# Optimization experiments

Hardware: AMD Instinct MI355X
Metric: run time of the kernel (lower is better)

The kernel has to match this reference:

```python
import jax, jax.numpy as jnp
import numpy as np

FP8_MAX = 448.0  # finfo(float8_e4m3fn).max
BLK = 128        # block_size = [128, 128]


def _quant_dequant_act(x):
    """Dynamic per-token, per-128-block fp8 quantization followed by dequant.
    Matches fp8_act_quant: scale = amax(block)/448, q = fp8(x/scale), deq = q*scale."""
    T, K = x.shape
    xb = x.reshape(T, K // BLK, BLK)
    amax = jnp.max(jnp.abs(xb), axis=-1, keepdims=True)
    scale = jnp.maximum(amax, 1e-12) / FP8_MAX  # [T, K//BLK, 1]
    q = (xb / scale).astype(jnp.float8_e4m3fn).astype(jnp.float32)
    return (q * scale).reshape(T, K)


def _dequant_weight(w, s):
    """Block-wise dequant of an fp8-valued [N, K] weight with [N//BLK, K//BLK] scales."""
    N, K = w.shape
    wb = w.reshape(N // BLK, BLK, K // BLK, BLK)
    return (wb * s[:, None, :, None]).reshape(N, K)


def setup_inputs() -> dict:
    key = jax.random.key(0)
    ks = jax.random.split(key, 7)
    T, H, I, E, TOPK = 8192, 2048, 1024, 32, 8
    f8 = lambda x: x.astype(jnp.float8_e4m3fn).astype(jnp.float32)  # store fp8-valued weights as f32
    hidden_states = jax.random.normal(ks[0], (T, H), jnp.float32)
    gate_up_proj = f8(jax.random.normal(ks[1], (E, 2 * I, H), jnp.float32))
    gate_up_proj_scale_inv = jax.random.uniform(ks[2], (E, (2 * I) // BLK, H // BLK), jnp.float32, 0.005, 0.02)
    down_proj = f8(jax.random.normal(ks[3], (E, H, I), jnp.float32))
    down_proj_scale_inv = jax.random.uniform(ks[4], (E, H // BLK, I // BLK), jnp.float32, 0.005, 0.02)
    top_k_index = jax.random.randint(ks[5], (T, TOPK), 0, E, jnp.int32)
    tw = jax.random.uniform(ks[6], (T, TOPK), jnp.float32)
    top_k_weights = tw / jnp.sum(tw, axis=-1, keepdims=True)
    return {
        'hidden_states': hidden_states,
        'gate_up_proj': gate_up_proj,
        'gate_up_proj_scale_inv': gate_up_proj_scale_inv,
        'down_proj': down_proj,
        'down_proj_scale_inv': down_proj_scale_inv,
        'top_k_weights': top_k_weights,
        'top_k_index': top_k_index,
    }


def reference(hidden_states, gate_up_proj, gate_up_proj_scale_inv, down_proj,
              down_proj_scale_inv, top_k_weights, top_k_index):
    E = gate_up_proj.shape[0]
    # Dynamic activation quantization is per-token (expert-independent): do it once.
    x_deq = _quant_dequant_act(hidden_states)  # [T, H]
    # Per-expert combine weight: cw[e, t] = sum_k top_k_weights[t,k] * (top_k_index[t,k]==e)
    hit = top_k_index[None, :, :] == jnp.arange(E, dtype=top_k_index.dtype)[:, None, None]
    cw = jnp.sum(jnp.where(hit, top_k_weights[None, :, :], 0.0), axis=-1)  # [E, T]

    def body(acc, xs):
        wgu, sgu, wd, sd, w_tok = xs
        h = x_deq @ _dequant_weight(wgu, sgu).T          # [T, 2I] fp8 grouped GEMM
        gate, up = jnp.split(h, 2, axis=-1)
        h = jax.nn.silu(gate) * up                        # _apply_gate
        h = _quant_dequant_act(h)                         # re-quantize before down_proj
        y = h @ _dequant_weight(wd, sd).T                 # [T, H]
        return acc + w_tok[:, None] * y, None

    acc0 = jnp.zeros_like(hidden_states, dtype=jnp.float32)
    out, _ = jax.lax.scan(
        body, acc0,
        (gate_up_proj, gate_up_proj_scale_inv, down_proj, down_proj_scale_inv, cw))
    return out
```

## Files before the change

### kernel.cpp

```cpp
#include <hip/hip_runtime.h>

typedef float f32x4 __attribute__((ext_vector_type(4)));
typedef float f32x16 __attribute__((ext_vector_type(16)));
typedef long long i64t;

constexpr int T = 8192, H = 2048, II = 1024, E = 32, TOPK = 8;
constexpr int NSLOT = T * TOPK;
constexpr int MT_MAX = 32;
constexpr int MT1 = 64;

__device__ __forceinline__ i64t frag8(const unsigned char* lds, int row, int kbyte) {
  int c8 = (kbyte >> 3) ^ ((row & 7) << 1) ^ ((row >> 3) & 1);
  return *(const i64t*)(lds + row * 128 + c8 * 8);
}
__device__ __forceinline__ void wr16c(unsigned char* lds, int r, int c, uint4 v) {
  if ((r >> 3) & 1) v = make_uint4(v.z, v.w, v.x, v.y);
  *(uint4*)(lds + r * 128 + ((c ^ (r & 7)) << 4)) = v;
}

__global__ void k_quant_x(const float* __restrict__ x, unsigned char* __restrict__ x8,
                          float* __restrict__ xs) {
  int gw = blockIdx.x * 4 + (threadIdx.x >> 6);
  int lane = threadIdx.x & 63;
  int token = gw >> 4, kb = gw & 15;
  float2 v = *(const float2*)(x + (size_t)token * H + kb * 128 + lane * 2);
  float am = fmaxf(fabsf(v.x), fabsf(v.y));
#pragma unroll
  for (int m = 1; m <= 32; m <<= 1) am = fmaxf(am, __shfl_xor(am, m, 64));
  float scale = fmaxf(am, 1e-12f) / 448.0f;
  int pk = __builtin_amdgcn_cvt_pk_fp8_f32(v.x / scale, v.y / scale, 0, false);
  *(unsigned short*)(x8 + (size_t)token * H + kb * 128 + lane * 2) = (unsigned short)(pk & 0xffff);
  if (lane == 0) xs[token * 16 + kb] = scale;
}

__global__ void k_cvt_w(const float* __restrict__ w, unsigned char* __restrict__ w8, int n4) {
  int i = blockIdx.x * 256 + threadIdx.x;
  if (i >= n4) return;
  f32x4 v = *(const f32x4*)(w + (size_t)i * 4);
  int p = __builtin_amdgcn_cvt_pk_fp8_f32(v[0], v[1], 0, false);
  p = __builtin_amdgcn_cvt_pk_fp8_f32(v[2], v[3], p, true);
  *(unsigned int*)(w8 + (size_t)i * 4) = (unsigned int)p;
}

__global__ void k_count(const int* __restrict__ tki, int* __restrict__ counts) {
  int i = blockIdx.x * 256 + threadIdx.x;
  if (i < NSLOT) atomicAdd(&counts[tki[i]], 1);
}
__global__ void k_scan(const int* __restrict__ counts, int* __restrict__ offsets) {
  if (threadIdx.x == 0) {
    int s = 0;
    for (int e = 0; e < E; ++e) { offsets[e] = s; s += counts[e]; }
    offsets[E] = s;
  }
}
__global__ void k_fill(const int* __restrict__ tki, const float* __restrict__ tkw,
                       const int* __restrict__ offsets, int* __restrict__ cursor,
                       int* __restrict__ tok_list, float* __restrict__ cw_list) {
  int i = blockIdx.x * 256 + threadIdx.x;
  if (i < NSLOT) {
    int e = tki[i];
    int pos = atomicAdd(&cursor[e], 1);
    int slot = offsets[e] + pos;
    tok_list[slot] = i >> 3;
    cw_list[slot] = tkw[i];
  }
}

__launch_bounds__(256, 2)
__global__ void k_gemm1(const unsigned char* __restrict__ x8, const float* __restrict__ xs,
                        const unsigned char* __restrict__ wgu8, const float* __restrict__ sgu,
                        const int* __restrict__ offsets, const int* __restrict__ tok_list,
                        unsigned char* __restrict__ a8, float* __restrict__ ascale) {
  __shared__ __align__(16) unsigned char lA[64 * 128];
  __shared__ __align__(16) unsigned char lBg[128 * 128];
  __shared__ __align__(16) unsigned char lBu[128 * 128];
  __shared__ float lsx[16 * 64];
  __shared__ int ltok[64];
  __shared__ float lamax[64 * 2];
  __shared__ float lscale[64];

  int bx = blockIdx.x;
  int e = bx >> 9, mt = (bx >> 3) & 63, nt = bx & 7;
  int off0 = offsets[e];
  int Me = offsets[e + 1] - off0;
  if (mt * 64 >= Me) return;
  int vrows = Me - mt * 64; if (vrows > 64) vrows = 64;
  int tid = threadIdx.x;

  if (tid < 64) ltok[tid] = (tid < vrows) ? tok_list[off0 + mt * 64 + tid] : -1;
  __syncthreads();

  if (tid < 128) {
    int r = tid >> 1, h = tid & 1;
    int tokr = ltok[r]; int tk = tokr < 0 ? 0 : tokr;
#pragma unroll
    for (int i = 0; i < 2; ++i) {
      f32x4 v = *(const f32x4*)(xs + (size_t)tk * 16 + h * 8 + i * 4);
#pragma unroll
      for (int j = 0; j < 4; ++j) lsx[(h * 8 + i * 4 + j) * 64 + r] = (tokr < 0) ? 0.0f : v[j];
    }
  }

  const int lane = tid & 63, wid = tid >> 6;
  const int wm = wid >> 1, wn = wid & 1;
  const int l31 = lane & 31, lg = lane >> 5;

  const int ra = tid >> 2, qa = tid & 3;
  const int rb = tid >> 1, hb = tid & 1;
  int tokA = ltok[ra] < 0 ? 0 : ltok[ra];
  const unsigned char* gA = x8 + (size_t)tokA * H + qa * 32;
  const unsigned char* gG = wgu8 + ((size_t)e * 2048 + nt * 128 + rb) * H + hb * 64;
  const unsigned char* gU = gG + (size_t)1024 * H;

  {
    uint4 a0 = *(const uint4*)gA, a1 = *(const uint4*)(gA + 16);
    uint4 g0 = *(const uint4*)gG, g1 = *(const uint4*)(gG + 16);
    uint4 g2 = *(const uint4*)(gG + 32), g3 = *(const uint4*)(gG + 48);
    uint4 u0 = *(const uint4*)gU, u1 = *(const uint4*)(gU + 16);
    uint4 u2 = *(const uint4*)(gU + 32), u3 = *(const uint4*)(gU + 48);
    wr16c(lA, ra, qa * 2 + 0, a0); wr16c(lA, ra, qa * 2 + 1, a1);
    wr16c(lBg, rb, hb * 4 + 0, g0); wr16c(lBg, rb, hb * 4 + 1, g1);
    wr16c(lBg, rb, hb * 4 + 2, g2); wr16c(lBg, rb, hb * 4 + 3, g3);
    wr16c(lBu, rb, hb * 4 + 0, u0); wr16c(lBu, rb, hb * 4 + 1, u1);
    wr16c(lBu, rb, hb * 4 + 2, u2); wr16c(lBu, rb, hb * 4 + 3, u3);
  }
  __syncthreads();

  f32x16 aG[2] = {};
  f32x16 aU[2] = {};

  for (int kb = 0; kb < 16; ++kb) {
    uint4 pA0, pA1, pG0, pG1, pG2, pG3, pU0, pU1, pU2, pU3;
    if (kb < 15) {
      pA0 = *(const uint4*)(gA + (kb + 1) * 128);
      pA1 = *(const uint4*)(gA + (kb + 1) * 128 + 16);
      pG0 = *(const uint4*)(gG + (kb + 1) * 128);
      pG1 = *(const uint4*)(gG + (kb + 1) * 128 + 16);
      pG2 = *(const uint4*)(gG + (kb + 1) * 128 + 32);
      pG3 = *(const uint4*)(gG + (kb + 1) * 128 + 48);
      pU0 = *(const uint4*)(gU + (kb + 1) * 128);
      pU1 = *(const uint4*)(gU + (kb + 1) * 128 + 16);
      pU2 = *(const uint4*)(gU + (kb + 1) * 128 + 32);
      pU3 = *(const uint4*)(gU + (kb + 1) * 128 + 48);
    }

    float swg = sgu[(e * 16 + nt) * 16 + kb];
    float swu = sgu[(e * 16 + 8 + nt) * 16 + kb];

    i64t af[8];
#pragma unroll
    for (int ks = 0; ks < 8; ++ks)
      af[ks] = frag8(lA, wm * 32 + l31, ks * 16 + lg * 8);
    f32x4 sxv[4];
#pragma unroll
    for (int jj = 0; jj < 4; ++jj)
      sxv[jj] = *(const f32x4*)(&lsx[kb * 64 + wm * 32 + jj * 8 + lg * 4]);

#pragma unroll
    for (int gu = 0; gu < 2; ++gu) {
      const unsigned char* lB = gu ? lBu : lBg;
      float sw = gu ? swu : swg;
#pragma unroll
      for (int nf = 0; nf < 2; ++nf) {
        i64t bf[8];
#pragma unroll
        for (int ks = 0; ks < 8; ++ks)
          bf[ks] = frag8(lB, wn * 64 + nf * 32 + l31, ks * 16 + lg * 8);
        f32x16 t = {};
#pragma unroll
        for (int ks = 0; ks < 8; ++ks)
          t = __builtin_amdgcn_mfma_f32_32x32x16_fp8_fp8(af[ks], bf[ks], t, 0, 0, 0);
#pragma unroll
        for (int j = 0; j < 16; ++j) {
          float f = sxv[j >> 2][j & 3] * sw;
          if (gu) aU[nf][j] += t[j] * f; else aG[nf][j] += t[j] * f;
        }
      }
    }

    if (kb < 15) {
      __syncthreads();
      wr16c(lA, ra, qa * 2 + 0, pA0); wr16c(lA, ra, qa * 2 + 1, pA1);
      wr16c(lBg, rb, hb * 4 + 0, pG0); wr16c(lBg, rb, hb * 4 + 1, pG1);
      wr16c(lBg, rb, hb * 4 + 2, pG2); wr16c(lBg, rb, hb * 4 + 3, pG3);
      wr16c(lBu, rb, hb * 4 + 0, pU0); wr16c(lBu, rb, hb * 4 + 1, pU1);
      wr16c(lBu, rb, hb * 4 + 2, pU2); wr16c(lBu, rb, hb * 4 + 3, pU3);
      __syncthreads();
    }
  }

#pragma unroll
  for (int nf = 0; nf < 2; ++nf)
#pragma unroll
    for (int j = 0; j < 16; ++j) {
      float g = aG[nf][j], u = aU[nf][j];
      aG[nf][j] = g * (1.0f / (1.0f + expf(-g))) * u;
    }

#pragma unroll
  for (int j = 0; j < 16; ++j) {
    float m = fmaxf(fabsf(aG[0][j]), fabsf(aG[1][j]));
#pragma unroll
    for (int msk = 1; msk <= 16; msk <<= 1) m = fmaxf(m, __shfl_xor(m, msk, 64));
    if (l31 == 0)
      lamax[(wm * 32 + (j & 3) + ((j >> 2) * 8) + lg * 4) * 2 + wn] = m;
  }
  __syncthreads();
  if (tid < 64) {
    float mm = fmaxf(lamax[tid * 2], lamax[tid * 2 + 1]);
    lscale[tid] = fmaxf(mm, 1e-12f) / 448.0f;
  }
  __syncthreads();

#pragma unroll
  for (int j = 0; j < 16; ++j) {
    int row = wm * 32 + (j & 3) + ((j >> 2) * 8) + lg * 4;
    float sc = lscale[row];
#pragma unroll
    for (int nf = 0; nf < 2; ++nf) {
      int pk = __builtin_amdgcn_cvt_pk_fp8_f32(aG[nf][j] / sc, 0.0f, 0, false);
      lA[row * 128 + wn * 64 + nf * 32 + l31] = (unsigned char)(pk & 0xff);
    }
    if (row < vrows && l31 == 0 && wn == 0)
      ascale[(off0 + mt * 64 + row) * 8 + nt] = sc;
  }
  __syncthreads();
#pragma unroll
  for (int it = 0; it < 2; ++it) {
    int idx = it * 256 + tid;
    int row = idx >> 3, c = idx & 7;
    if (row < vrows)
      *(uint4*)(a8 + (size_t)(off0 + mt * 64 + row) * 1024 + nt * 128 + c * 16) =
          *(const uint4*)(lA + row * 128 + c * 16);
  }
}

__launch_bounds__(256, 2)
__global__ void k_gemm2(const unsigned char* __restrict__ a8, const float* __restrict__ ascale,
                        const unsigned char* __restrict__ wd8, const float* __restrict__ sd,
                        const int* __restrict__ offsets, const int* __restrict__ tok_list,
                        const float* __restrict__ cw_list, float* __restrict__ out) {
  __shared__ __align__(16) unsigned char lA[128 * 128];
  __shared__ __align__(16) unsigned char lB[128 * 128];
  __shared__ float las[8 * 128];
  __shared__ int ltok[128];
  __shared__ float lcw[128];

  int bx = blockIdx.x;
  int e = bx >> 9, mt = (bx >> 4) & 31, nt = bx & 15;
  int off0 = offsets[e];
  int Me = offsets[e + 1] - off0;
  if (mt * 128 >= Me) return;
  int vrows = Me - mt * 128; if (vrows > 128) vrows = 128;
  int tid = threadIdx.x;

  if (tid < 128) {
    bool v = tid < vrows;
    ltok[tid] = v ? tok_list[off0 + mt * 128 + tid] : 0;
    lcw[tid] = v ? cw_list[off0 + mt * 128 + tid] : 0.0f;
  }
  int r = tid >> 1, h = tid & 1;
  int srow = off0 + mt * 128 + r; if (srow > NSLOT - 1) srow = NSLOT - 1;
  {
    f32x4 v = *(const f32x4*)(ascale + (size_t)srow * 8 + h * 4);
#pragma unroll
    for (int j = 0; j < 4; ++j) las[(h * 4 + j) * 128 + r] = v[j];
  }

  const int lane = tid & 63, wid = tid >> 6;
  const int wm = wid >> 1, wn = wid & 1;
  const int l31 = lane & 31, lg = lane >> 5;

  const unsigned char* gA = a8 + (size_t)srow * 1024 + h * 64;
  const unsigned char* gB = wd8 + ((size_t)e * 2048 + nt * 128 + r) * 1024 + h * 64;

  uint4 rA[4], rB[4];
#pragma unroll
  for (int i = 0; i < 4; ++i) { rA[i] = ((const uint4*)gA)[i]; rB[i] = ((const uint4*)gB)[i]; }
#pragma unroll
  for (int i = 0; i < 4; ++i) { wr16c(lA, r, h * 4 + i, rA[i]); wr16c(lB, r, h * 4 + i, rB[i]); }
  __syncthreads();

  f32x16 acc[2][2] = {};

  for (int kb = 0; kb < 8; ++kb) {
    if (kb < 7) {
#pragma unroll
      for (int i = 0; i < 4; ++i) {
        rA[i] = ((const uint4*)(gA + (kb + 1) * 128))[i];
        rB[i] = ((const uint4*)(gB + (kb + 1) * 128))[i];
      }
    }
    float swd = sd[(e * 16 + nt) * 8 + kb];
    i64t bf[2][8];
#pragma unroll
    for (int nf = 0; nf < 2; ++nf)
#pragma unroll
      for (int ks = 0; ks < 8; ++ks)
        bf[nf][ks] = frag8(lB, wn * 64 + nf * 32 + l31, ks * 16 + lg * 8);
#pragma unroll
    for (int mf = 0; mf < 2; ++mf) {
      i64t af[8];
#pragma unroll
      for (int ks = 0; ks < 8; ++ks)
        af[ks] = frag8(lA, wm * 64 + mf * 32 + l31, ks * 16 + lg * 8);
      f32x4 sav[4];
#pragma unroll
      for (int jj = 0; jj < 4; ++jj)
        sav[jj] = *(const f32x4*)(&las[kb * 128 + wm * 64 + mf * 32 + jj * 8 + lg * 4]);
#pragma unroll
      for (int nf = 0; nf < 2; ++nf) {
        f32x16 t = {};
#pragma unroll
        for (int ks = 0; ks < 8; ++ks)
          t = __builtin_amdgcn_mfma_f32_32x32x16_fp8_fp8(af[ks], bf[nf][ks], t, 0, 0, 0);
#pragma unroll
        for (int j = 0; j < 16; ++j)
          acc[mf][nf][j] += t[j] * (sav[j >> 2][j & 3] * swd);
      }
    }
    if (kb < 7) {
      __syncthreads();
#pragma unroll
      for (int i = 0; i < 4; ++i) { wr16c(lA, r, h * 4 + i, rA[i]); wr16c(lB, r, h * 4 + i, rB[i]); }
      __syncthreads();
    }
  }

#pragma unroll
  for (int mf = 0; mf < 2; ++mf)
#pragma unroll
    for (int j = 0; j < 16; ++j) {
      int row = wm * 64 + mf * 32 + (j & 3) + ((j >> 2) * 8) + lg * 4;
      if (row < vrows) {
        int token = ltok[row];
        float w = lcw[row];
#pragma unroll
        for (int nf = 0; nf < 2; ++nf)
          unsafeAtomicAdd(out + (size_t)token * 2048 + nt * 128 + wn * 64 + nf * 32 + l31,
                          acc[mf][nf][j] * w);
      }
    }
}

extern "C" void kernel_launch(void* const* d_in, const int* in_sizes, int n_in,
                              void* d_out, int out_size, void* d_ws, size_t ws_size,
                              hipStream_t stream) {
  const float* x   = (const float*)d_in[0];
  const float* wgu = (const float*)d_in[1];
  const float* sgu = (const float*)d_in[2];
  const float* wd  = (const float*)d_in[3];
  const float* sd  = (const float*)d_in[4];
  const float* tkw = (const float*)d_in[5];
  const int*   tki = (const int*)d_in[6];
  float* out = (float*)d_out;

  char* ws = (char*)d_ws;
  size_t o = 0;
  auto alloc = [&](size_t sz) { void* p = ws + o; o = (o + sz + 255) & ~(size_t)255; return p; };
  unsigned char* x8    = (unsigned char*)alloc((size_t)T * H);
  unsigned char* wgu8  = (unsigned char*)alloc((size_t)E * 2 * II * H);
  unsigned char* wd8   = (unsigned char*)alloc((size_t)E * H * II);
  unsigned char* a8    = (unsigned char*)alloc((size_t)NSLOT * II);
  float* xs            = (float*)alloc((size_t)T * 16 * 4);
  float* as_           = (float*)alloc((size_t)NSLOT * 8 * 4);
  int* counts          = (int*)alloc(128);
  int* cursor          = (int*)alloc(128);
  int* offsets         = (int*)alloc(256);
  int* tok_list        = (int*)alloc((size_t)NSLOT * 4);
  float* cw_list       = (float*)alloc((size_t)NSLOT * 4);

  hipMemsetAsync(counts, 0, 128, stream);
  hipMemsetAsync(cursor, 0, 128, stream);
  hipMemsetAsync(d_out, 0, (size_t)out_size * 4, stream);

  k_quant_x<<<dim3((T * 16) / 4), dim3(256), 0, stream>>>(x, x8, xs);
  k_cvt_w<<<dim3((E * 2 * II * H / 4) / 256), dim3(256), 0, stream>>>(wgu, wgu8, E * 2 * II * H / 4);
  k_cvt_w<<<dim3((E * H * II / 4) / 256), dim3(256), 0, stream>>>(wd, wd8, E * H * II / 4);
  k_count<<<dim3(NSLOT / 256), dim3(256), 0, stream>>>(tki, counts);
  k_scan<<<dim3(1), dim3(64), 0, stream>>>(counts, offsets);
  k_fill<<<dim3(NSLOT / 256), dim3(256), 0, stream>>>(tki, tkw, offsets, cursor, tok_list, cw_list);
  k_gemm1<<<dim3(E * MT1 * 8), dim3(256), 0, stream>>>(x8, xs, wgu8, sgu, offsets, tok_list, a8, as_);
  k_gemm2<<<dim3(E * MT_MAX * 16), dim3(256), 0, stream>>>(a8, as_, wd8, sd, offsets, tok_list, cw_list, out);
}
```

Before: 1.712 ms.

## Replace atomic scatter-add in down-proj with per-slot stores plus gather reduce

Instead of atomically adding each expert's weighted output into the token output, the second GEMM writes each slot's weighted result to a dense per-slot buffer. A new reduce kernel then gathers each token's eight slot rows via a recorded slot index and writes the output directly, which also removes the output memset. This trades float atomics for an extra large buffer of roughly half a gigabyte written and read back. It falls back to the atomic path if the workspace is too small.

```diff
diff --git a/kernel.cpp b/kernel.cpp
--- a/kernel.cpp
+++ b/kernel.cpp
@@ -55,7 +55,8 @@
 }
 __global__ void k_fill(const int* __restrict__ tki, const float* __restrict__ tkw,
                        const int* __restrict__ offsets, int* __restrict__ cursor,
-                       int* __restrict__ tok_list, float* __restrict__ cw_list) {
+                       int* __restrict__ tok_list, float* __restrict__ cw_list,
+                       int* __restrict__ islot) {
   int i = blockIdx.x * 256 + threadIdx.x;
   if (i < NSLOT) {
     int e = tki[i];
@@ -63,6 +64,7 @@
     int slot = offsets[e] + pos;
     tok_list[slot] = i >> 3;
     cw_list[slot] = tkw[i];
+    islot[i] = slot;
   }
 }
 
@@ -235,11 +237,13 @@
   }
 }
 
+template <bool USE_SLOT>
 __launch_bounds__(256, 2)
-__global__ void k_gemm2(const unsigned char* __restrict__ a8, const float* __restrict__ ascale,
-                        const unsigned char* __restrict__ wd8, const float* __restrict__ sd,
-                        const int* __restrict__ offsets, const int* __restrict__ tok_list,
-                        const float* __restrict__ cw_list, float* __restrict__ out) {
+__global__ void k_gemm2_t(const unsigned char* __restrict__ a8, const float* __restrict__ ascale,
+                          const unsigned char* __restrict__ wd8, const float* __restrict__ sd,
+                          const int* __restrict__ offsets, const int* __restrict__ tok_list,
+                          const float* __restrict__ cw_list, float* __restrict__ out,
+                          float* __restrict__ yslot) {
   __shared__ __align__(16) unsigned char lA[128 * 128];
   __shared__ __align__(16) unsigned char lB[128 * 128];
   __shared__ float las[8 * 128];
@@ -333,14 +337,35 @@
     for (int j = 0; j < 16; ++j) {
       int row = wm * 64 + mf * 32 + (j & 3) + ((j >> 2) * 8) + lg * 4;
       if (row < vrows) {
-        int token = ltok[row];
         float w = lcw[row];
-#pragma unroll
-        for (int nf = 0; nf < 2; ++nf)
-          unsafeAtomicAdd(out + (size_t)token * 2048 + nt * 128 + wn * 64 + nf * 32 + l31,
-                          acc[mf][nf][j] * w);
+        if (USE_SLOT) {
+          size_t s = (size_t)(off0 + mt * 128 + row) * 2048 + nt * 128;
+#pragma unroll
+          for (int nf = 0; nf < 2; ++nf)
+            yslot[s + wn * 64 + nf * 32 + l31] = acc[mf][nf][j] * w;
+        } else {
+          int token = ltok[row];
+#pragma unroll
+          for (int nf = 0; nf < 2; ++nf)
+            unsafeAtomicAdd(out + (size_t)token * 2048 + nt * 128 + wn * 64 + nf * 32 + l31,
+                            acc[mf][nf][j] * w);
+        }
       }
     }
+}
+
+__global__ void k_reduce(const float* __restrict__ yslot, const int* __restrict__ islot,
+                         float* __restrict__ out) {
+  __shared__ int ls[8];
+  int t = blockIdx.x >> 1;
+  int c = ((blockIdx.x & 1) << 8) + threadIdx.x;
+  if (threadIdx.x < 8) ls[threadIdx.x] = islot[t * 8 + threadIdx.x];
+  __syncthreads();
+  f32x4 s = {};
+#pragma unroll
+  for (int k = 0; k < 8; ++k)
+    s += *(const f32x4*)(yslot + (size_t)ls[k] * 2048 + c * 4);
+  *(f32x4*)(out + (size_t)t * 2048 + c * 4) = s;
 }
 
 extern "C" void kernel_launch(void* const* d_in, const int* in_sizes, int n_in,
@@ -369,17 +394,27 @@
   int* offsets         = (int*)alloc(256);
   int* tok_list        = (int*)alloc((size_t)NSLOT * 4);
   float* cw_list       = (float*)alloc((size_t)NSLOT * 4);
+  int* islot           = (int*)alloc((size_t)NSLOT * 4);
+  float* yslot         = (float*)alloc((size_t)NSLOT * H * 4);
+  bool use_slot = (o <= ws_size);
 
   hipMemsetAsync(counts, 0, 128, stream);
   hipMemsetAsync(cursor, 0, 128, stream);
-  hipMemsetAsync(d_out, 0, (size_t)out_size * 4, stream);
+  if (!use_slot) hipMemsetAsync(d_out, 0, (size_t)out_size * 4, stream);
 
   k_quant_x<<<dim3((T * 16) / 4), dim3(256), 0, stream>>>(x, x8, xs);
   k_cvt_w<<<dim3((E * 2 * II * H / 4) / 256), dim3(256), 0, stream>>>(wgu, wgu8, E * 2 * II * H / 4);
   k_cvt_w<<<dim3((E * H * II / 4) / 256), dim3(256), 0, stream>>>(wd, wd8, E * H * II / 4);
   k_count<<<dim3(NSLOT / 256), dim3(256), 0, stream>>>(tki, counts);
   k_scan<<<dim3(1), dim3(64), 0, stream>>>(counts, offsets);
-  k_fill<<<dim3(NSLOT / 256), dim3(256), 0, stream>>>(tki, tkw, offsets, cursor, tok_list, cw_list);
+  k_fill<<<dim3(NSLOT / 256), dim3(256), 0, stream>>>(tki, tkw, offsets, cursor, tok_list, cw_list, islot);
   k_gemm1<<<dim3(E * MT1 * 8), dim3(256), 0, stream>>>(x8, xs, wgu8, sgu, offsets, tok_list, a8, as_);
-  k_gemm2<<<dim3(E * MT_MAX * 16), dim3(256), 0, stream>>>(a8, as_, wd8, sd, offsets, tok_list, cw_list, out);
-}
+  if (use_slot) {
+    k_gemm2_t<true><<<dim3(E * MT_MAX * 16), dim3(256), 0, stream>>>(
+        a8, as_, wd8, sd, offsets, tok_list, cw_list, out, yslot);
+    k_reduce<<<dim3(T * 2), dim3(256), 0, stream>>>(yslot, islot, out);
+  } else {
+    k_gemm2_t<false><<<dim3(E * MT_MAX * 16), dim3(256), 0, stream>>>(
+        a8, as_, wd8, sd, offsets, tok_list, cw_list, out, yslot);
+  }
+}
```

New measurement: 1.715 ms. Within noise of the previous version (+0.2%).

## Replace gemm2 scatter atomics with fp16 per-slot staging and gather reduce

Applied to the files above, without the earlier changes.

The down-projection kernel no longer atomically adds each weighted row into the output. It writes the weighted rows as fp16 into a per-slot buffer that reuses the fp8 gate_up weight workspace, and a new reduce kernel sums the 8 slot rows of each token in fp32. The N dimension is split into two halves so the staging buffer fits in that workspace, and the output memset is removed. This trades contended global float atomics for extra launches and staging traffic, and rounding the partial results to fp16 before summation adds precision loss.

```diff
diff --git a/kernel.cpp b/kernel.cpp
--- a/kernel.cpp
+++ b/kernel.cpp
@@ -2,6 +2,7 @@
 
 typedef float f32x4 __attribute__((ext_vector_type(4)));
 typedef float f32x16 __attribute__((ext_vector_type(16)));
+typedef _Float16 f16x4 __attribute__((ext_vector_type(4)));
 typedef long long i64t;
 
 constexpr int T = 8192, H = 2048, II = 1024, E = 32, TOPK = 8;
@@ -55,7 +56,8 @@
 }
 __global__ void k_fill(const int* __restrict__ tki, const float* __restrict__ tkw,
                        const int* __restrict__ offsets, int* __restrict__ cursor,
-                       int* __restrict__ tok_list, float* __restrict__ cw_list) {
+                       int* __restrict__ tok_list, float* __restrict__ cw_list,
+                       int* __restrict__ islot) {
   int i = blockIdx.x * 256 + threadIdx.x;
   if (i < NSLOT) {
     int e = tki[i];
@@ -63,6 +65,7 @@
     int slot = offsets[e] + pos;
     tok_list[slot] = i >> 3;
     cw_list[slot] = tkw[i];
+    islot[i] = slot;
   }
 }
 
@@ -238,27 +241,24 @@
 __launch_bounds__(256, 2)
 __global__ void k_gemm2(const unsigned char* __restrict__ a8, const float* __restrict__ ascale,
                         const unsigned char* __restrict__ wd8, const float* __restrict__ sd,
-                        const int* __restrict__ offsets, const int* __restrict__ tok_list,
-                        const float* __restrict__ cw_list, float* __restrict__ out) {
-  __shared__ __align__(16) unsigned char lA[128 * 128];
-  __shared__ __align__(16) unsigned char lB[128 * 128];
+                        const int* __restrict__ offsets, const float* __restrict__ cw_list,
+                        int ntbase, _Float16* __restrict__ yslot) {
+  __shared__ __align__(16) unsigned char lbuf[2][128 * 128];
+  unsigned char* lA = lbuf[0];
+  unsigned char* lB = lbuf[1];
   __shared__ float las[8 * 128];
-  __shared__ int ltok[128];
   __shared__ float lcw[128];
 
   int bx = blockIdx.x;
-  int e = bx >> 9, mt = (bx >> 4) & 31, nt = bx & 15;
+  int e = bx >> 8, mt = (bx >> 3) & 31, nth = bx & 7;
+  int nt = ntbase + nth;
   int off0 = offsets[e];
   int Me = offsets[e + 1] - off0;
   if (mt * 128 >= Me) return;
   int vrows = Me - mt * 128; if (vrows > 128) vrows = 128;
   int tid = threadIdx.x;
 
-  if (tid < 128) {
-    bool v = tid < vrows;
-    ltok[tid] = v ? tok_list[off0 + mt * 128 + tid] : 0;
-    lcw[tid] = v ? cw_list[off0 + mt * 128 + tid] : 0.0f;
-  }
+  if (tid < 128) lcw[tid] = (tid < vrows) ? cw_list[off0 + mt * 128 + tid] : 0.0f;
   int r = tid >> 1, h = tid & 1;
   int srow = off0 + mt * 128 + r; if (srow > NSLOT - 1) srow = NSLOT - 1;
   {
@@ -327,20 +327,44 @@
     }
   }
 
+  __syncthreads();
+  _Float16* lh = (_Float16*)lbuf;
 #pragma unroll
   for (int mf = 0; mf < 2; ++mf)
 #pragma unroll
     for (int j = 0; j < 16; ++j) {
       int row = wm * 64 + mf * 32 + (j & 3) + ((j >> 2) * 8) + lg * 4;
-      if (row < vrows) {
-        int token = ltok[row];
-        float w = lcw[row];
-#pragma unroll
-        for (int nf = 0; nf < 2; ++nf)
-          unsafeAtomicAdd(out + (size_t)token * 2048 + nt * 128 + wn * 64 + nf * 32 + l31,
-                          acc[mf][nf][j] * w);
-      }
-    }
+      float w = lcw[row];
+#pragma unroll
+      for (int nf = 0; nf < 2; ++nf)
+        lh[row * 128 + wn * 64 + nf * 32 + l31] = (_Float16)(acc[mf][nf][j] * w);
+    }
+  __syncthreads();
+#pragma unroll
+  for (int it = 0; it < 8; ++it) {
+    int idx = it * 256 + tid;
+    int row = idx >> 4, u = idx & 15;
+    if (row < vrows)
+      *(uint4*)((char*)yslot + ((size_t)(off0 + mt * 128 + row) * 1024 + nth * 128) * 2 + u * 16) =
+          *(const uint4*)((const char*)lh + row * 256 + u * 16);
+  }
+}
+
+__global__ void k_reduce(const _Float16* __restrict__ yslot, const int* __restrict__ islot,
+                         float* __restrict__ out, int half) {
+  __shared__ int ls[8];
+  int t = blockIdx.x;
+  if (threadIdx.x < 8) ls[threadIdx.x] = islot[t * 8 + threadIdx.x];
+  __syncthreads();
+  int c = threadIdx.x * 4;
+  float s0 = 0, s1 = 0, s2 = 0, s3 = 0;
+#pragma unroll
+  for (int k = 0; k < 8; ++k) {
+    f16x4 v = *(const f16x4*)(yslot + (size_t)ls[k] * 1024 + c);
+    s0 += (float)v[0]; s1 += (float)v[1]; s2 += (float)v[2]; s3 += (float)v[3];
+  }
+  f32x4 r = {s0, s1, s2, s3};
+  *(f32x4*)(out + (size_t)t * 2048 + half * 1024 + c) = r;
 }
 
 extern "C" void kernel_launch(void* const* d_in, const int* in_sizes, int n_in,
@@ -369,17 +393,21 @@
   int* offsets         = (int*)alloc(256);
   int* tok_list        = (int*)alloc((size_t)NSLOT * 4);
   float* cw_list       = (float*)alloc((size_t)NSLOT * 4);
+  int* islot           = (int*)alloc((size_t)NSLOT * 4);
+  _Float16* yslot      = (_Float16*)wgu8;
 
   hipMemsetAsync(counts, 0, 128, stream);
   hipMemsetAsync(cursor, 0, 128, stream);
-  hipMemsetAsync(d_out, 0, (size_t)out_size * 4, stream);
 
   k_quant_x<<<dim3((T * 16) / 4), dim3(256), 0, stream>>>(x, x8, xs);
   k_cvt_w<<<dim3((E * 2 * II * H / 4) / 256), dim3(256), 0, stream>>>(wgu, wgu8, E * 2 * II * H / 4);
   k_cvt_w<<<dim3((E * H * II / 4) / 256), dim3(256), 0, stream>>>(wd, wd8, E * H * II / 4);
   k_count<<<dim3(NSLOT / 256), dim3(256), 0, stream>>>(tki, counts);
   k_scan<<<dim3(1), dim3(64), 0, stream>>>(counts, offsets);
-  k_fill<<<dim3(NSLOT / 256), dim3(256), 0, stream>>>(tki, tkw, offsets, cursor, tok_list, cw_list);
+  k_fill<<<dim3(NSLOT / 256), dim3(256), 0, stream>>>(tki, tkw, offsets, cursor, tok_list, cw_list, islot);
   k_gemm1<<<dim3(E * MT1 * 8), dim3(256), 0, stream>>>(x8, xs, wgu8, sgu, offsets, tok_list, a8, as_);
-  k_gemm2<<<dim3(E * MT_MAX * 16), dim3(256), 0, stream>>>(a8, as_, wd8, sd, offsets, tok_list, cw_list, out);
-}
+  k_gemm2<<<dim3(E * MT_MAX * 8), dim3(256), 0, stream>>>(a8, as_, wd8, sd, offsets, cw_list, 0, yslot);
+  k_reduce<<<dim3(T), dim3(256), 0, stream>>>(yslot, islot, out, 0);
+  k_gemm2<<<dim3(E * MT_MAX * 8), dim3(256), 0, stream>>>(a8, as_, wd8, sd, offsets, cw_list, 8, yslot);
+  k_reduce<<<dim3(T), dim3(256), 0, stream>>>(yslot, islot, out, 1);
+}
```

New measurement: 1.590 ms, median of 2. -7.1%, faster.
